# Optimization experiments

Measured on AMD Instinct MI355X. Metric: run time of the kernel, lower is better.

Reference implementation:

```python
import jax, jax.numpy as jnp
import numpy as np

NUM_TOKENS = 8192
DIM = 256
BETA = 0.25
DECAY = 0.99
EPS = 1e-05


def setup_inputs() -> dict:
    key = jax.random.key(0)
    k1, k2 = jax.random.split(key, 2)
    z = jax.random.normal(k1, (16, DIM, 32, 32), dtype=jnp.float32)
    embedding = jax.random.normal(k2, (NUM_TOKENS, DIM), dtype=jnp.float32)
    cluster_size = jnp.zeros((NUM_TOKENS,), dtype=jnp.float32)
    ema_w = embedding  # module init copies embed_init into both embedding and ema_w
    return {"z": z, "embedding": embedding, "cluster_size": cluster_size, "ema_w": ema_w}


def reference(z, embedding, cluster_size, ema_w):
    # z: [B, D, H, W] -> [B, H, W, D]
    zp = jnp.transpose(z, (0, 2, 3, 1))
    zf = zp.reshape(-1, DIM)  # [N, D]
    # squared euclidean distances [N, K] via ||z||^2 + ||e||^2 - 2 z.e
    d = (jnp.sum(zf * zf, axis=1, keepdims=True)
         + jnp.sum(embedding * embedding, axis=1)
         - 2.0 * (zf @ embedding.T))
    idx = jnp.argmin(d, axis=1)  # [N]
    z_q = embedding[idx].reshape(zp.shape)  # [B, H, W, D]

    # training-mode EMA statistics (pure-functional: returned as new states)
    counts = jax.ops.segment_sum(jnp.ones(zf.shape[0], dtype=zf.dtype), idx,
                                 num_segments=NUM_TOKENS)
    embed_sum = jax.ops.segment_sum(zf, idx, num_segments=NUM_TOKENS)  # [K, D]
    cs = cluster_size * DECAY + (1.0 - DECAY) * counts
    new_ema_w = ema_w * DECAY + (1.0 - DECAY) * embed_sum
    # torch evaluates sum AFTER add_(eps): denom = sum(cs + eps) + K*eps
    cs = cs + EPS
    new_cluster_size = cs / (jnp.sum(cs) + NUM_TOKENS * EPS)
    new_embedding = new_ema_w / new_cluster_size[:, None]

    loss = BETA * jnp.mean((jax.lax.stop_gradient(z_q) - zp) ** 2)
    # straight-through estimator
    z_q_st = zp + jax.lax.stop_gradient(z_q - zp)
    out = jnp.transpose(z_q_st, (0, 3, 1, 2))  # back to [B, D, H, W]
    return out, loss, idx, new_cluster_size, new_ema_w, new_embedding
```

## Files before the change

### kernel.cpp

```cpp
#include <hip/hip_runtime.h>

#define N_TOK   16384
#define K_CODES 8192
#define DIMS    256
#define MARGIN  0.25f

#define OUT_OFF  0
#define LOSS_OFF 4194304
#define IDX_OFF  4194305
#define NCS_OFF  4210689
#define NEMA_OFF 4218881
#define NEMB_OFF 6316033

#define WS_ZFRAG  0u
#define WS_EFRAG  16777216u
#define WS_ENORM  25165824u
#define WS_CNT    25198592u
#define WS_CS     25231360u
#define WS_OFFS   25264128u
#define WS_WPOS   25296896u
#define WS_TLIST  25329664u
#define WS_IDXI   25395200u
#define WS_GCNT   25460736u
#define WS_DENOM  25526272u
#define WS_GCAND  25526784u

typedef _Float16 f16x8 __attribute__((ext_vector_type(8)));
typedef float    f32x16 __attribute__((ext_vector_type(16)));

union HU { _Float16 h; unsigned short u; };

static __device__ inline void split_f32(float x, unsigned short& hi, unsigned short& lo) {
    HU a; a.h = (_Float16)x;
    float r = (x - (float)a.h) * 2048.0f;
    HU b; b.h = (_Float16)r;
    hi = a.u; lo = b.u;
}

static __device__ inline float join_f16(unsigned short h, unsigned short l) {
    HU a, b; a.u = h; b.u = l;
    return (float)a.h + (float)b.h * 4.8828125e-4f;
}

#define GLD16(gp, lp) __builtin_amdgcn_global_load_lds( \
    (const __attribute__((address_space(1))) unsigned int*)(gp), \
    (__attribute__((address_space(3))) unsigned int*)(lp), 16, 0, 0)

__global__ __launch_bounds__(256) void cvt_z_kernel(const float* __restrict__ z,
                                                    unsigned short* __restrict__ zfrag,
                                                    float* __restrict__ loss_cell,
                                                    double* __restrict__ denom) {
    __shared__ float T[64][65];
    const int t = threadIdx.x;
    const int hg = blockIdx.x & 15, dg = (blockIdx.x >> 4) & 3, b = blockIdx.x >> 6;
    if (blockIdx.x == 0 && t == 0) { *loss_cell = 0.f; *denom = 0.0; }
    const int c4 = (t & 15) * 4, r0 = t >> 4;
    const float* zb = z + (((size_t)(b * 256 + dg * 64)) << 10) + hg * 64;
#pragma unroll
    for (int p = 0; p < 4; ++p) {
        const int r = r0 + p * 16;
        const float4 v = *(const float4*)(zb + ((size_t)r << 10) + c4);
        T[r][c4] = v.x; T[r][c4 + 1] = v.y; T[r][c4 + 2] = v.z; T[r][c4 + 3] = v.w;
    }
    __syncthreads();
    const int tr = t & 63, dc = (t >> 6) * 16;
    const int tile = b * 16 + hg;
    const int tg = tile * 2 + (tr >> 5), l31 = tr & 31;
    const int ks = dg * 4 + (dc >> 4);
    unsigned short hb[16], lb[16];
#pragma unroll
    for (int j = 0; j < 16; ++j) split_f32(T[dc + j][tr], hb[j], lb[j]);
#pragma unroll
    for (int lv = 0; lv < 2; ++lv) {
        const unsigned short* src = lv ? lb : hb;
        unsigned short* dst = zfrag + (size_t)((tg * 2 + lv) * 16 + ks) * 512;
        *(uint4*)(dst + l31 * 8)       = ((const uint4*)src)[0];
        *(uint4*)(dst + 256 + l31 * 8) = ((const uint4*)src)[1];
    }
}

__global__ __launch_bounds__(256) void cvt_e_enorm(const float* __restrict__ emb,
                                                   unsigned short* __restrict__ efrag,
                                                   float* __restrict__ enorm,
                                                   int* __restrict__ cnt,
                                                   int* __restrict__ gcnt) {
    __shared__ double red[256];
    const int t = threadIdx.x, g = blockIdx.x;
    const int lane = t & 63, q = t >> 6;
    const int l31 = lane & 31, lhi = lane >> 5;
    if (g < 32) cnt[g * 256 + t] = 0;
    if (g < 64) gcnt[g * 256 + t] = 0;
    const float* rowp = emb + (size_t)(g * 32 + l31) * 256 + lhi * 8;
    double s = 0.0;
#pragma unroll
    for (int kk = 0; kk < 4; ++kk) {
        const int ks = q * 4 + kk;
        const float4 a = *(const float4*)(rowp + ks * 16);
        const float4 bq = *(const float4*)(rowp + ks * 16 + 4);
        const float vv[8] = {a.x, a.y, a.z, a.w, bq.x, bq.y, bq.z, bq.w};
        unsigned short hb[8], lb[8];
#pragma unroll
        for (int j = 0; j < 8; ++j) {
            split_f32(vv[j], hb[j], lb[j]);
            s += (double)vv[j] * (double)vv[j];
        }
        *(uint4*)(efrag + (size_t)((g * 2 + 0) * 16 + ks) * 512 + lane * 8) = *(const uint4*)hb;
        *(uint4*)(efrag + (size_t)((g * 2 + 1) * 16 + ks) * 512 + lane * 8) = *(const uint4*)lb;
    }
    red[t] = s;
    __syncthreads();
    if (t < 32) {
        double acc = 0.0;
#pragma unroll
        for (int qq = 0; qq < 4; ++qq) acc += red[qq * 64 + t] + red[qq * 64 + 32 + t];
        enorm[g * 32 + t] = (float)acc;
    }
}

__global__ __launch_bounds__(256, 2) void argmin_approx(
    const unsigned short* __restrict__ zfrag, const unsigned short* __restrict__ efrag,
    const float* __restrict__ enorm, int* __restrict__ gcnt,
    unsigned short* __restrict__ gcand) {
    __shared__ __align__(16) unsigned short E[2][4096];
    __shared__ float en_s[2][64];
    __shared__ unsigned short lcand[128][32];
    __shared__ int lcnt[128];

    const int tid = threadIdx.x, lane = tid & 63, wave = tid >> 6;
    const int tile = blockIdx.x >> 2, csplit = blockIdx.x & 3;
    const int token0 = tile * 128, code0 = csplit * 2048;

    if (tid < 128) lcnt[tid] = 0;

    f16x8 Zr[16];
    {
        const unsigned short* zb = zfrag + (size_t)(tile * 4 + wave) * 16384 + lane * 8;
#pragma unroll
        for (int ks = 0; ks < 16; ++ks) Zr[ks] = *(const f16x8*)(zb + ks * 512);
    }

#pragma unroll
    for (int cg = 0; cg < 2; ++cg)
        GLD16(efrag + ((size_t)(csplit * 64 + cg) * 32 + wave) * 512 + lane * 8,
              &E[0][(cg * 4 + wave) * 512]);
    if (tid < 64) en_s[0][tid] = enorm[code0 + tid];
    __syncthreads();

    float bv = 3.4e38f;

    for (int ct = 0; ct < 32; ++ct) {
        f32x16 acc[2];
#pragma unroll
        for (int cg = 0; cg < 2; ++cg)
#pragma unroll
            for (int qq = 0; qq < 16; ++qq) acc[cg][qq] = 0.f;

#pragma unroll
        for (int kc = 0; kc < 4; ++kc) {
            const int p = (ct * 4 + kc) & 1;
            if (!(ct == 31 && kc == 3)) {
                const int nch = ct * 4 + kc + 1;
                const int nct = nch >> 2, nkc = nch & 3;
#pragma unroll
                for (int cg = 0; cg < 2; ++cg)
                    GLD16(efrag + ((size_t)(csplit * 64 + nct * 2 + cg) * 32 + nkc * 4 + wave) * 512 + lane * 8,
                          &E[p ^ 1][(cg * 4 + wave) * 512]);
            }
            if (kc == 0 && ct < 31 && tid < 64)
                en_s[(ct + 1) & 1][tid] = enorm[code0 + (ct + 1) * 64 + tid];

#pragma unroll
            for (int ksl = 0; ksl < 4; ++ksl) {
                const f16x8 ae0 = *(const f16x8*)&E[p][(0 * 4 + ksl) * 512 + lane * 8];
                const f16x8 ae1 = *(const f16x8*)&E[p][(1 * 4 + ksl) * 512 + lane * 8];
                acc[0] = __builtin_amdgcn_mfma_f32_32x32x16_f16(ae0, Zr[kc * 4 + ksl], acc[0], 0, 0, 0);
                acc[1] = __builtin_amdgcn_mfma_f32_32x32x16_f16(ae1, Zr[kc * 4 + ksl], acc[1], 0, 0, 0);
            }
            if (kc == 3) {
                const int rbase = 4 * (lane >> 5);
                const float* ens = en_s[ct & 1];
#pragma unroll
                for (int cg = 0; cg < 2; ++cg)
#pragma unroll
                    for (int r = 0; r < 16; ++r) {
                        const int cl = cg * 32 + (r & 3) + 8 * (r >> 2) + rbase;
                        const float sv = ens[cl] - 2.0f * acc[cg][r];
                        acc[cg][r] = sv;
                        if (sv < bv) bv = sv;
                    }
                const float ob = __shfl_xor(bv, 32);
                const float thr = fminf(bv, ob) + MARGIN;
                const int tl = wave * 32 + (lane & 31);
#pragma unroll
                for (int cg = 0; cg < 2; ++cg)
#pragma unroll
                    for (int r = 0; r < 16; ++r)
                        if (acc[cg][r] < thr) {
                            const int cl = cg * 32 + (r & 3) + 8 * (r >> 2) + rbase;
                            const int code = code0 + ct * 64 + cl;
                            const int pp = atomicAdd(&lcnt[tl], 1);
                            if (pp < 32) lcand[tl][pp] = (unsigned short)code;
                            else {
                                const int gp = atomicAdd(&gcnt[token0 + tl], 1);
                                if (gp < 64) gcand[(size_t)(token0 + tl) * 64 + gp] = (unsigned short)code;
                            }
                        }
            }
            __syncthreads();
        }
    }
    if (lane < 32) {
        const int tl = wave * 32 + lane;
        const int token = token0 + tl;
        const int L = min(lcnt[tl], 32);
        const int base = atomicAdd(&gcnt[token], L);
        for (int i = 0; i < L; ++i) {
            const int gp = base + i;
            if (gp < 64) gcand[(size_t)token * 64 + gp] = lcand[tl][i];
        }
    }
}

__global__ __launch_bounds__(256) void rescore_kernel(
    const unsigned short* __restrict__ zfrag, const unsigned short* __restrict__ efrag,
    const float* __restrict__ enorm, const int* __restrict__ gcnt,
    const unsigned short* __restrict__ gcand, int* __restrict__ idx_i,
    float* __restrict__ idx_f, int* __restrict__ cnt) {
    const int lane = threadIdx.x & 63, wave = threadIdx.x >> 6;
    const int t = blockIdx.x * 4 + wave;
    const int ks = lane >> 2, khalf = (lane >> 1) & 1, j0 = (lane & 1) * 4;
    const int loff = khalf * 256 + j0;
    const int tg = t >> 5, tl = t & 31;
    float zf[4];
    {
        const ushort4 hv = *(const ushort4*)(zfrag + (size_t)((tg * 2 + 0) * 16 + ks) * 512 + loff + tl * 8);
        const ushort4 lv = *(const ushort4*)(zfrag + (size_t)((tg * 2 + 1) * 16 + ks) * 512 + loff + tl * 8);
        const unsigned short* hp = (const unsigned short*)&hv;
        const unsigned short* lp = (const unsigned short*)&lv;
#pragma unroll
        for (int j = 0; j < 4; ++j) zf[j] = join_f16(hp[j], lp[j]);
    }
    const int C = min(gcnt[t], 64);
    float best = 3.4e38f; int besti = 0;
    for (int i = 0; i < C; ++i) {
        const int c = gcand[(size_t)t * 64 + i];
        const int g = c >> 5, cl = c & 31;
        const ushort4 he = *(const ushort4*)(efrag + (size_t)((g * 2 + 0) * 16 + ks) * 512 + loff + cl * 8);
        const ushort4 le = *(const ushort4*)(efrag + (size_t)((g * 2 + 1) * 16 + ks) * 512 + loff + cl * 8);
        const unsigned short* hp = (const unsigned short*)&he;
        const unsigned short* lp = (const unsigned short*)&le;
        float dot = 0.f;
#pragma unroll
        for (int j = 0; j < 4; ++j) dot += zf[j] * join_f16(hp[j], lp[j]);
#pragma unroll
        for (int off = 32; off; off >>= 1) dot += __shfl_xor(dot, off);
        const float s = enorm[c] - 2.0f * dot;
        if (s < best || (s == best && c < besti)) { best = s; besti = c; }
    }
    if (lane == 0) {
        idx_i[t] = besti;
        idx_f[t] = (float)besti;
        atomicAdd(&cnt[besti], 1);
    }
}

__global__ __launch_bounds__(256) void scan_kernel(const int* __restrict__ cnt,
                                                   int* __restrict__ offs,
                                                   int* __restrict__ wpos) {
    __shared__ int part[256];
    const int tid = threadIdx.x;
    const int base = tid * 32;
    int loc[32];
    int s = 0;
#pragma unroll
    for (int j = 0; j < 32; ++j) { loc[j] = cnt[base + j]; s += loc[j]; }
    part[tid] = s;
    __syncthreads();
    for (int off = 1; off < 256; off <<= 1) {
        int v = 0;
        if (tid >= off) v = part[tid - off];
        __syncthreads();
        if (tid >= off) part[tid] += v;
        __syncthreads();
    }
    int run = (tid > 0) ? part[tid - 1] : 0;
#pragma unroll
    for (int j = 0; j < 32; ++j) {
        offs[base + j] = run;
        wpos[base + j] = run;
        run += loc[j];
    }
}

__global__ __launch_bounds__(256) void scatter_cs(
    const int* __restrict__ idx_i, int* __restrict__ wpos, int* __restrict__ tlist,
    const float* __restrict__ cluster_size, const int* __restrict__ cnt,
    float* __restrict__ cs, double* __restrict__ denom) {
    __shared__ double red[256];
    const int t = threadIdx.x, b = blockIdx.x;
    if (b < 64) {
        const int n = b * 256 + t;
        const int k = idx_i[n];
        tlist[atomicAdd(&wpos[k], 1)] = n;
    } else {
        const int k = (b - 64) * 256 + t;
        const float v = cluster_size[k] * 0.99f + 0.01f * (float)cnt[k] + 1e-5f;
        cs[k] = v;
        red[t] = (double)v;
        __syncthreads();
        for (int s2 = 128; s2; s2 >>= 1) {
            if (t < s2) red[t] += red[t + s2];
            __syncthreads();
        }
        if (t == 0) atomicAdd(denom, red[0]);
    }
}

__global__ __launch_bounds__(256) void nema_gather(
    const unsigned short* __restrict__ zfrag,
    const int* __restrict__ offs, const int* __restrict__ cnt, const int* __restrict__ tlist,
    const float* __restrict__ ema_w, const float* __restrict__ cs,
    const double* __restrict__ denom, float* __restrict__ ncs_out,
    float* __restrict__ nema_out, float* __restrict__ nemb_out,
    const float* __restrict__ z, const float* __restrict__ emb,
    const int* __restrict__ idx_i, float* __restrict__ out, float* __restrict__ loss_cell) {
    __shared__ float redf[256];
    const int t = threadIdx.x;
    if (blockIdx.x < 2048) {
        const int lane = t & 63, wave = t >> 6;
        const int k = blockIdx.x * 4 + wave;
        const int l31 = lane & 31, sel = lane >> 5;
        const int beg = offs[k], c = cnt[k];
        float acc[8] = {0.f, 0.f, 0.f, 0.f, 0.f, 0.f, 0.f, 0.f};
        for (int i = 0; i < c; ++i) {
            const int tok = tlist[beg + i];
            const int tg = tok >> 5, tl = tok & 31;
            const uint4 v = *(const uint4*)(zfrag +
                (size_t)((tg * 2 + sel) * 16 + (l31 >> 1)) * 512 + (l31 & 1) * 256 + tl * 8);
            uint4 o;
            o.x = __shfl_xor((int)v.x, 32); o.y = __shfl_xor((int)v.y, 32);
            o.z = __shfl_xor((int)v.z, 32); o.w = __shfl_xor((int)v.w, 32);
            if (lane < 32) {
                const unsigned short* hp = (const unsigned short*)&v;
                const unsigned short* lp = (const unsigned short*)&o;
#pragma unroll
                for (int j = 0; j < 8; ++j) acc[j] += join_f16(hp[j], lp[j]);
            }
        }
        const float dn = (float)(*denom) + (float)K_CODES * 1e-5f;
        const float ncs = cs[k] / dn;
        if (lane == 0) ncs_out[k] = ncs;
        if (lane < 32) {
            const size_t off = ((size_t)k << 8) + l31 * 8;
#pragma unroll
            for (int j = 0; j < 8; ++j) {
                const float ne = ema_w[off + j] * 0.99f + 0.01f * acc[j];
                nema_out[off + j] = ne;
                nemb_out[off + j] = ne / ncs;
            }
        }
    } else {
        const int gb = blockIdx.x - 2048;
        const int n0 = (gb >> 2) * 64;
        const int dg = (gb & 3) * 64;
        const int b = n0 >> 10, hw0 = n0 & 1023;
        const int lane = t & 63, w = t >> 6;
        const int n = n0 + lane;
        const int k = idx_i[n];
        const float* zb = z + ((size_t)b << 18) + hw0 + lane;
        float* ob = out + ((size_t)b << 18) + hw0 + lane;
        float ls = 0.f;
#pragma unroll 4
        for (int d = dg + w; d < dg + 64; d += 4) {
            const float zv = zb[(size_t)d << 10];
            const float ev = emb[((size_t)k << 8) + d];
            ob[(size_t)d << 10] = ev;
            const float df = ev - zv;
            ls += df * df;
        }
        redf[t] = ls;
        __syncthreads();
        for (int s2 = 128; s2; s2 >>= 1) {
            if (t < s2) redf[t] += redf[t + s2];
            __syncthreads();
        }
        if (t == 0) atomicAdd(loss_cell, redf[0] * (0.25f / 4194304.0f));
    }
}

extern "C" void kernel_launch(void* const* d_in, const int* in_sizes, int n_in,
                              void* d_out, int out_size, void* d_ws, size_t ws_size,
                              hipStream_t stream) {
    const float* z            = (const float*)d_in[0];
    const float* emb          = (const float*)d_in[1];
    const float* cluster_size = (const float*)d_in[2];
    const float* ema_w        = (const float*)d_in[3];
    float* out = (float*)d_out;
    char*  wsb = (char*)d_ws;

    unsigned short* zfrag = (unsigned short*)(wsb + WS_ZFRAG);
    unsigned short* efrag = (unsigned short*)(wsb + WS_EFRAG);
    float*  enorm  = (float*)(wsb + WS_ENORM);
    int*    cnt    = (int*)(wsb + WS_CNT);
    float*  cs     = (float*)(wsb + WS_CS);
    int*    offs   = (int*)(wsb + WS_OFFS);
    int*    wpos   = (int*)(wsb + WS_WPOS);
    int*    tlist  = (int*)(wsb + WS_TLIST);
    int*    idx_i  = (int*)(wsb + WS_IDXI);
    int*    gcnt   = (int*)(wsb + WS_GCNT);
    double* denom  = (double*)(wsb + WS_DENOM);
    unsigned short* gcand = (unsigned short*)(wsb + WS_GCAND);

    cvt_z_kernel<<<1024, 256, 0, stream>>>(z, zfrag, out + LOSS_OFF, denom);
    cvt_e_enorm<<<256, 256, 0, stream>>>(emb, efrag, enorm, cnt, gcnt);
    argmin_approx<<<512, 256, 0, stream>>>(zfrag, efrag, enorm, gcnt, gcand);
    rescore_kernel<<<4096, 256, 0, stream>>>(zfrag, efrag, enorm, gcnt, gcand,
                                             idx_i, out + IDX_OFF, cnt);
    scan_kernel<<<1, 256, 0, stream>>>(cnt, offs, wpos);
    scatter_cs<<<96, 256, 0, stream>>>(idx_i, wpos, tlist, cluster_size, cnt, cs, denom);
    nema_gather<<<3072, 256, 0, stream>>>(zfrag, offs, cnt, tlist, ema_w, cs, denom,
                                          out + NCS_OFF, out + NEMA_OFF, out + NEMB_OFF,
                                          z, emb, idx_i, out + OUT_OFF, out + LOSS_OFF);
}
```

Baseline: 433.5 us.

## Fuse conversion kernels, widen argmin staging, split rescore across waves, vectorize gather

Merges the z and embedding conversion kernels into one launch. Changes argmin staging from 4 barriers per 64-code tile to one full-K tile per barrier with 64KB double-buffered LDS, which may lower occupancy. Rescore now gives each token a whole block, with 4 waves splitting the candidates and a shared-memory reduction. The output gather reads the embedding as float4 and uses twice as many blocks.

Result: slower. 445.4 us (+2.7%).

```diff
diff --git a/kernel.cpp b/kernel.cpp
--- a/kernel.cpp
+++ b/kernel.cpp
@@ -46,74 +46,71 @@
     (const __attribute__((address_space(1))) unsigned int*)(gp), \
     (__attribute__((address_space(3))) unsigned int*)(lp), 16, 0, 0)
 
-__global__ __launch_bounds__(256) void cvt_z_kernel(const float* __restrict__ z,
-                                                    unsigned short* __restrict__ zfrag,
-                                                    float* __restrict__ loss_cell,
-                                                    double* __restrict__ denom) {
-    __shared__ float T[64][65];
+__global__ __launch_bounds__(256) void cvt_all(
+    const float* __restrict__ z, unsigned short* __restrict__ zfrag,
+    const float* __restrict__ emb, unsigned short* __restrict__ efrag,
+    float* __restrict__ enorm, int* __restrict__ cnt, int* __restrict__ gcnt,
+    float* __restrict__ loss_cell, double* __restrict__ denom) {
     const int t = threadIdx.x;
-    const int hg = blockIdx.x & 15, dg = (blockIdx.x >> 4) & 3, b = blockIdx.x >> 6;
-    if (blockIdx.x == 0 && t == 0) { *loss_cell = 0.f; *denom = 0.0; }
-    const int c4 = (t & 15) * 4, r0 = t >> 4;
-    const float* zb = z + (((size_t)(b * 256 + dg * 64)) << 10) + hg * 64;
-#pragma unroll
-    for (int p = 0; p < 4; ++p) {
-        const int r = r0 + p * 16;
-        const float4 v = *(const float4*)(zb + ((size_t)r << 10) + c4);
-        T[r][c4] = v.x; T[r][c4 + 1] = v.y; T[r][c4 + 2] = v.z; T[r][c4 + 3] = v.w;
-    }
-    __syncthreads();
-    const int tr = t & 63, dc = (t >> 6) * 16;
-    const int tile = b * 16 + hg;
-    const int tg = tile * 2 + (tr >> 5), l31 = tr & 31;
-    const int ks = dg * 4 + (dc >> 4);
-    unsigned short hb[16], lb[16];
-#pragma unroll
-    for (int j = 0; j < 16; ++j) split_f32(T[dc + j][tr], hb[j], lb[j]);
-#pragma unroll
-    for (int lv = 0; lv < 2; ++lv) {
-        const unsigned short* src = lv ? lb : hb;
-        unsigned short* dst = zfrag + (size_t)((tg * 2 + lv) * 16 + ks) * 512;
-        *(uint4*)(dst + l31 * 8)       = ((const uint4*)src)[0];
-        *(uint4*)(dst + 256 + l31 * 8) = ((const uint4*)src)[1];
-    }
-}
-
-__global__ __launch_bounds__(256) void cvt_e_enorm(const float* __restrict__ emb,
-                                                   unsigned short* __restrict__ efrag,
-                                                   float* __restrict__ enorm,
-                                                   int* __restrict__ cnt,
-                                                   int* __restrict__ gcnt) {
-    __shared__ double red[256];
-    const int t = threadIdx.x, g = blockIdx.x;
-    const int lane = t & 63, q = t >> 6;
-    const int l31 = lane & 31, lhi = lane >> 5;
-    if (g < 32) cnt[g * 256 + t] = 0;
-    if (g < 64) gcnt[g * 256 + t] = 0;
-    const float* rowp = emb + (size_t)(g * 32 + l31) * 256 + lhi * 8;
-    double s = 0.0;
-#pragma unroll
-    for (int kk = 0; kk < 4; ++kk) {
-        const int ks = q * 4 + kk;
-        const float4 a = *(const float4*)(rowp + ks * 16);
-        const float4 bq = *(const float4*)(rowp + ks * 16 + 4);
-        const float vv[8] = {a.x, a.y, a.z, a.w, bq.x, bq.y, bq.z, bq.w};
-        unsigned short hb[8], lb[8];
-#pragma unroll
-        for (int j = 0; j < 8; ++j) {
-            split_f32(vv[j], hb[j], lb[j]);
-            s += (double)vv[j] * (double)vv[j];
-        }
-        *(uint4*)(efrag + (size_t)((g * 2 + 0) * 16 + ks) * 512 + lane * 8) = *(const uint4*)hb;
-        *(uint4*)(efrag + (size_t)((g * 2 + 1) * 16 + ks) * 512 + lane * 8) = *(const uint4*)lb;
-    }
-    red[t] = s;
-    __syncthreads();
-    if (t < 32) {
-        double acc = 0.0;
-#pragma unroll
-        for (int qq = 0; qq < 4; ++qq) acc += red[qq * 64 + t] + red[qq * 64 + 32 + t];
-        enorm[g * 32 + t] = (float)acc;
+    if (blockIdx.x < 1024) {
+        __shared__ float T[64][65];
+        const int hg = blockIdx.x & 15, dg = (blockIdx.x >> 4) & 3, b = blockIdx.x >> 6;
+        if (blockIdx.x == 0 && t == 0) { *loss_cell = 0.f; *denom = 0.0; }
+        const int c4 = (t & 15) * 4, r0 = t >> 4;
+        const float* zb = z + (((size_t)(b * 256 + dg * 64)) << 10) + hg * 64;
+#pragma unroll
+        for (int p = 0; p < 4; ++p) {
+            const int r = r0 + p * 16;
+            const float4 v = *(const float4*)(zb + ((size_t)r << 10) + c4);
+            T[r][c4] = v.x; T[r][c4 + 1] = v.y; T[r][c4 + 2] = v.z; T[r][c4 + 3] = v.w;
+        }
+        __syncthreads();
+        const int tr = t & 63, dc = (t >> 6) * 16;
+        const int tile = b * 16 + hg;
+        const int tg = tile * 2 + (tr >> 5), l31 = tr & 31;
+        const int ks = dg * 4 + (dc >> 4);
+        unsigned short hb[16], lb[16];
+#pragma unroll
+        for (int j = 0; j < 16; ++j) split_f32(T[dc + j][tr], hb[j], lb[j]);
+#pragma unroll
+        for (int lv = 0; lv < 2; ++lv) {
+            const unsigned short* src = lv ? lb : hb;
+            unsigned short* dst = zfrag + (size_t)((tg * 2 + lv) * 16 + ks) * 512;
+            *(uint4*)(dst + l31 * 8)       = ((const uint4*)src)[0];
+            *(uint4*)(dst + 256 + l31 * 8) = ((const uint4*)src)[1];
+        }
+    } else {
+        __shared__ double red[256];
+        const int g = blockIdx.x - 1024;
+        const int lane = t & 63, q = t >> 6;
+        const int l31 = lane & 31, lhi = lane >> 5;
+        if (g < 32) cnt[g * 256 + t] = 0;
+        if (g < 64) gcnt[g * 256 + t] = 0;
+        const float* rowp = emb + (size_t)(g * 32 + l31) * 256 + lhi * 8;
+        double s = 0.0;
+#pragma unroll
+        for (int kk = 0; kk < 4; ++kk) {
+            const int ks = q * 4 + kk;
+            const float4 a = *(const float4*)(rowp + ks * 16);
+            const float4 bq = *(const float4*)(rowp + ks * 16 + 4);
+            const float vv[8] = {a.x, a.y, a.z, a.w, bq.x, bq.y, bq.z, bq.w};
+            unsigned short hb[8], lb[8];
+#pragma unroll
+            for (int j = 0; j < 8; ++j) {
+                split_f32(vv[j], hb[j], lb[j]);
+                s += (double)vv[j] * (double)vv[j];
+            }
+            *(uint4*)(efrag + (size_t)((g * 2 + 0) * 16 + ks) * 512 + lane * 8) = *(const uint4*)hb;
+            *(uint4*)(efrag + (size_t)((g * 2 + 1) * 16 + ks) * 512 + lane * 8) = *(const uint4*)lb;
+        }
+        red[t] = s;
+        __syncthreads();
+        if (t < 32) {
+            double acc = 0.0;
+#pragma unroll
+            for (int qq = 0; qq < 4; ++qq) acc += red[qq * 64 + t] + red[qq * 64 + 32 + t];
+            enorm[g * 32 + t] = (float)acc;
+        }
     }
 }
 
@@ -121,7 +118,7 @@
     const unsigned short* __restrict__ zfrag, const unsigned short* __restrict__ efrag,
     const float* __restrict__ enorm, int* __restrict__ gcnt,
     unsigned short* __restrict__ gcand) {
-    __shared__ __align__(16) unsigned short E[2][4096];
+    __shared__ __align__(16) unsigned short E2[2][16384];
     __shared__ float en_s[2][64];
     __shared__ unsigned short lcand[128][32];
     __shared__ int lcnt[128];
@@ -140,74 +137,68 @@
     }
 
 #pragma unroll
-    for (int cg = 0; cg < 2; ++cg)
-        GLD16(efrag + ((size_t)(csplit * 64 + cg) * 32 + wave) * 512 + lane * 8,
-              &E[0][(cg * 4 + wave) * 512]);
+    for (int i = 0; i < 8; ++i) {
+        const int slot = wave * 8 + i, cg = slot >> 4, ks = slot & 15;
+        const int g = csplit * 64 + cg;
+        GLD16(efrag + ((size_t)g * 32 + ks) * 512 + lane * 8, &E2[0][slot * 512]);
+    }
     if (tid < 64) en_s[0][tid] = enorm[code0 + tid];
     __syncthreads();
 
     float bv = 3.4e38f;
 
     for (int ct = 0; ct < 32; ++ct) {
+        const int p = ct & 1;
+        if (ct < 31) {
+#pragma unroll
+            for (int i = 0; i < 8; ++i) {
+                const int slot = wave * 8 + i, cg = slot >> 4, ks = slot & 15;
+                const int g = csplit * 64 + (ct + 1) * 2 + cg;
+                GLD16(efrag + ((size_t)g * 32 + ks) * 512 + lane * 8, &E2[p ^ 1][slot * 512]);
+            }
+            if (tid < 64) en_s[(ct + 1) & 1][tid] = enorm[code0 + (ct + 1) * 64 + tid];
+        }
         f32x16 acc[2];
 #pragma unroll
         for (int cg = 0; cg < 2; ++cg)
 #pragma unroll
             for (int qq = 0; qq < 16; ++qq) acc[cg][qq] = 0.f;
-
-#pragma unroll
-        for (int kc = 0; kc < 4; ++kc) {
-            const int p = (ct * 4 + kc) & 1;
-            if (!(ct == 31 && kc == 3)) {
-                const int nch = ct * 4 + kc + 1;
-                const int nct = nch >> 2, nkc = nch & 3;
-#pragma unroll
-                for (int cg = 0; cg < 2; ++cg)
-                    GLD16(efrag + ((size_t)(csplit * 64 + nct * 2 + cg) * 32 + nkc * 4 + wave) * 512 + lane * 8,
-                          &E[p ^ 1][(cg * 4 + wave) * 512]);
+#pragma unroll
+        for (int ks = 0; ks < 16; ++ks) {
+            const f16x8 ae0 = *(const f16x8*)&E2[p][(0 * 16 + ks) * 512 + lane * 8];
+            const f16x8 ae1 = *(const f16x8*)&E2[p][(1 * 16 + ks) * 512 + lane * 8];
+            acc[0] = __builtin_amdgcn_mfma_f32_32x32x16_f16(ae0, Zr[ks], acc[0], 0, 0, 0);
+            acc[1] = __builtin_amdgcn_mfma_f32_32x32x16_f16(ae1, Zr[ks], acc[1], 0, 0, 0);
+        }
+        const int rbase = 4 * (lane >> 5);
+        const float* ens = en_s[ct & 1];
+#pragma unroll
+        for (int cg = 0; cg < 2; ++cg)
+#pragma unroll
+            for (int r = 0; r < 16; ++r) {
+                const int cl = cg * 32 + (r & 3) + 8 * (r >> 2) + rbase;
+                const float sv = ens[cl] - 2.0f * acc[cg][r];
+                acc[cg][r] = sv;
+                if (sv < bv) bv = sv;
             }
-            if (kc == 0 && ct < 31 && tid < 64)
-                en_s[(ct + 1) & 1][tid] = enorm[code0 + (ct + 1) * 64 + tid];
-
-#pragma unroll
-            for (int ksl = 0; ksl < 4; ++ksl) {
-                const f16x8 ae0 = *(const f16x8*)&E[p][(0 * 4 + ksl) * 512 + lane * 8];
-                const f16x8 ae1 = *(const f16x8*)&E[p][(1 * 4 + ksl) * 512 + lane * 8];
-                acc[0] = __builtin_amdgcn_mfma_f32_32x32x16_f16(ae0, Zr[kc * 4 + ksl], acc[0], 0, 0, 0);
-                acc[1] = __builtin_amdgcn_mfma_f32_32x32x16_f16(ae1, Zr[kc * 4 + ksl], acc[1], 0, 0, 0);
-            }
-            if (kc == 3) {
-                const int rbase = 4 * (lane >> 5);
-                const float* ens = en_s[ct & 1];
-#pragma unroll
-                for (int cg = 0; cg < 2; ++cg)
-#pragma unroll
-                    for (int r = 0; r < 16; ++r) {
-                        const int cl = cg * 32 + (r & 3) + 8 * (r >> 2) + rbase;
-                        const float sv = ens[cl] - 2.0f * acc[cg][r];
-                        acc[cg][r] = sv;
-                        if (sv < bv) bv = sv;
+        const float ob = __shfl_xor(bv, 32);
+        const float thr = fminf(bv, ob) + MARGIN;
+        const int tl = wave * 32 + (lane & 31);
+#pragma unroll
+        for (int cg = 0; cg < 2; ++cg)
+#pragma unroll
+            for (int r = 0; r < 16; ++r)
+                if (acc[cg][r] < thr) {
+                    const int cl = cg * 32 + (r & 3) + 8 * (r >> 2) + rbase;
+                    const int code = code0 + ct * 64 + cl;
+                    const int pp = atomicAdd(&lcnt[tl], 1);
+                    if (pp < 32) lcand[tl][pp] = (unsigned short)code;
+                    else {
+                        const int gp = atomicAdd(&gcnt[token0 + tl], 1);
+                        if (gp < 64) gcand[(size_t)(token0 + tl) * 64 + gp] = (unsigned short)code;
                     }
-                const float ob = __shfl_xor(bv, 32);
-                const float thr = fminf(bv, ob) + MARGIN;
-                const int tl = wave * 32 + (lane & 31);
-#pragma unroll
-                for (int cg = 0; cg < 2; ++cg)
-#pragma unroll
-                    for (int r = 0; r < 16; ++r)
-                        if (acc[cg][r] < thr) {
-                            const int cl = cg * 32 + (r & 3) + 8 * (r >> 2) + rbase;
-                            const int code = code0 + ct * 64 + cl;
-                            const int pp = atomicAdd(&lcnt[tl], 1);
-                            if (pp < 32) lcand[tl][pp] = (unsigned short)code;
-                            else {
-                                const int gp = atomicAdd(&gcnt[token0 + tl], 1);
-                                if (gp < 64) gcand[(size_t)(token0 + tl) * 64 + gp] = (unsigned short)code;
-                            }
-                        }
-            }
-            __syncthreads();
-        }
+                }
+        __syncthreads();
     }
     if (lane < 32) {
         const int tl = wave * 32 + lane;
@@ -226,8 +217,10 @@
     const float* __restrict__ enorm, const int* __restrict__ gcnt,
     const unsigned short* __restrict__ gcand, int* __restrict__ idx_i,
     float* __restrict__ idx_f, int* __restrict__ cnt) {
+    __shared__ float redv[4];
+    __shared__ int   redi[4];
     const int lane = threadIdx.x & 63, wave = threadIdx.x >> 6;
-    const int t = blockIdx.x * 4 + wave;
+    const int t = blockIdx.x;
     const int ks = lane >> 2, khalf = (lane >> 1) & 1, j0 = (lane & 1) * 4;
     const int loff = khalf * 256 + j0;
     const int tg = t >> 5, tl = t & 31;
@@ -242,7 +235,7 @@
     }
     const int C = min(gcnt[t], 64);
     float best = 3.4e38f; int besti = 0;
-    for (int i = 0; i < C; ++i) {
+    for (int i = wave; i < C; i += 4) {
         const int c = gcand[(size_t)t * 64 + i];
         const int g = c >> 5, cl = c & 31;
         const ushort4 he = *(const ushort4*)(efrag + (size_t)((g * 2 + 0) * 16 + ks) * 512 + loff + cl * 8);
@@ -257,10 +250,16 @@
         const float s = enorm[c] - 2.0f * dot;
         if (s < best || (s == best && c < besti)) { best = s; besti = c; }
     }
-    if (lane == 0) {
-        idx_i[t] = besti;
-        idx_f[t] = (float)besti;
-        atomicAdd(&cnt[besti], 1);
+    if (lane == 0) { redv[wave] = best; redi[wave] = besti; }
+    __syncthreads();
+    if (threadIdx.x == 0) {
+        float bb = redv[0]; int bi2 = redi[0];
+#pragma unroll
+        for (int w2 = 1; w2 < 4; ++w2)
+            if (redv[w2] < bb || (redv[w2] == bb && redi[w2] < bi2)) { bb = redv[w2]; bi2 = redi[w2]; }
+        idx_i[t] = bi2;
+        idx_f[t] = (float)bi2;
+        atomicAdd(&cnt[bi2], 1);
     }
 }
 
@@ -361,21 +360,23 @@
         }
     } else {
         const int gb = blockIdx.x - 2048;
-        const int n0 = (gb >> 2) * 64;
-        const int dg = (gb & 3) * 64;
+        const int n0 = (gb >> 4) * 64;
+        const int lane = t & 63, w = t >> 6;
+        const int d4 = (gb & 15) * 16 + w * 4;
         const int b = n0 >> 10, hw0 = n0 & 1023;
-        const int lane = t & 63, w = t >> 6;
         const int n = n0 + lane;
         const int k = idx_i[n];
+        const float4 ef = *(const float4*)&emb[((size_t)k << 8) + d4];
+        const float ev[4] = {ef.x, ef.y, ef.z, ef.w};
         const float* zb = z + ((size_t)b << 18) + hw0 + lane;
         float* ob = out + ((size_t)b << 18) + hw0 + lane;
         float ls = 0.f;
-#pragma unroll 4
-        for (int d = dg + w; d < dg + 64; d += 4) {
+#pragma unroll
+        for (int j = 0; j < 4; ++j) {
+            const int d = d4 + j;
             const float zv = zb[(size_t)d << 10];
-            const float ev = emb[((size_t)k << 8) + d];
-            ob[(size_t)d << 10] = ev;
-            const float df = ev - zv;
+            ob[(size_t)d << 10] = ev[j];
+            const float df = ev[j] - zv;
             ls += df * df;
         }
         redf[t] = ls;
@@ -411,14 +412,14 @@
     double* denom  = (double*)(wsb + WS_DENOM);
     unsigned short* gcand = (unsigned short*)(wsb + WS_GCAND);
 
-    cvt_z_kernel<<<1024, 256, 0, stream>>>(z, zfrag, out + LOSS_OFF, denom);
-    cvt_e_enorm<<<256, 256, 0, stream>>>(emb, efrag, enorm, cnt, gcnt);
+    cvt_all<<<1280, 256, 0, stream>>>(z, zfrag, emb, efrag, enorm, cnt, gcnt,
+                                      out + LOSS_OFF, denom);
     argmin_approx<<<512, 256, 0, stream>>>(zfrag, efrag, enorm, gcnt, gcand);
-    rescore_kernel<<<4096, 256, 0, stream>>>(zfrag, efrag, enorm, gcnt, gcand,
-                                             idx_i, out + IDX_OFF, cnt);
+    rescore_kernel<<<16384, 256, 0, stream>>>(zfrag, efrag, enorm, gcnt, gcand,
+                                              idx_i, out + IDX_OFF, cnt);
     scan_kernel<<<1, 256, 0, stream>>>(cnt, offs, wpos);
     scatter_cs<<<96, 256, 0, stream>>>(idx_i, wpos, tlist, cluster_size, cnt, cs, denom);
-    nema_gather<<<3072, 256, 0, stream>>>(zfrag, offs, cnt, tlist, ema_w, cs, denom,
+    nema_gather<<<6144, 256, 0, stream>>>(zfrag, offs, cnt, tlist, ema_w, cs, denom,
                                           out + NCS_OFF, out + NEMA_OFF, out + NEMB_OFF,
                                           z, emb, idx_i, out + OUT_OFF, out + LOSS_OFF);
 }
```
